# Performance work log

Hardware: AMD Instinct MI355X
Metric: run time of the kernel (lower is better)

The kernel has to match this reference:

```python
import jax, jax.numpy as jnp
import numpy as np

EMBED_DIM = 1024
NUM_HEADS = 16
HEAD_DIM = EMBED_DIM // NUM_HEADS


def setup_inputs() -> dict:
    key = jax.random.key(0)
    ks = jax.random.split(key, 9)
    s = 1.0 / np.sqrt(EMBED_DIM)
    inp = {"x": jax.random.normal(ks[0], (2, 2048, EMBED_DIM), dtype=jnp.float32)}
    for i, name in enumerate(["q", "k", "v", "out"]):
        inp[f"W_{name}"] = jax.random.uniform(ks[1 + 2 * i], (EMBED_DIM, EMBED_DIM), jnp.float32, -s, s)
        inp[f"b_{name}"] = jax.random.uniform(ks[2 + 2 * i], (EMBED_DIM,), jnp.float32, -s, s)
    return inp


def _heads(x):
    # [B, S, D] -> [B, H, S, Dh]
    b, s, _ = x.shape
    return x.reshape(b, s, NUM_HEADS, HEAD_DIM).transpose(0, 2, 1, 3)


def reference(x, W_q, b_q, W_k, b_k, W_v, b_v, W_out, b_out):
    q = _heads(x @ W_q.T + b_q)
    k = _heads(x @ W_k.T + b_k)
    v = _heads(x @ W_v.T + b_v)
    scale = HEAD_DIM ** 0.5
    logits = jnp.einsum("bhqd,bhkd->bhqk", q, k) / scale  # [B,H,S,S]
    s = x.shape[1]
    causal = jnp.tril(jnp.ones((s, s), dtype=bool))
    logits = jnp.where(causal, logits, -jnp.inf)
    a = jax.nn.softmax(logits, axis=-1)
    o = jnp.einsum("bhqk,bhkd->bhqd", a, v)
    o = o.transpose(0, 2, 1, 3).reshape(x.shape[0], s, EMBED_DIM)
    return o @ W_out.T + b_out
```

## Files before the change

### kernel.cpp

```cpp
#include <hip/hip_runtime.h>
#include <hip/hip_bf16.h>

typedef __bf16 bf16_t;
typedef __bf16 bf16x8 __attribute__((ext_vector_type(8)));
typedef __bf16 bf16x4 __attribute__((ext_vector_type(4)));
typedef float  f32x4  __attribute__((ext_vector_type(4)));

#define MFMA16(a, b, c) __builtin_amdgcn_mfma_f32_16x16x32_bf16((a), (b), (c), 0, 0, 0)

constexpr int E  = 1024;
constexpr int S  = 2048;
constexpr int H  = 16;
constexpr int M  = 4096;

__device__ __forceinline__ void glds16(const bf16_t* src, bf16_t* dst) {
  __builtin_amdgcn_global_load_lds(
      (const __attribute__((address_space(1))) void*)src,
      (__attribute__((address_space(3))) void*)dst, 16, 0, 0);
}

template <int ROWS, int NT>
__device__ __forceinline__ void stage_tile(const bf16_t* g, int gld,
                                           bf16_t* lds, int tid) {
  const int w = tid >> 6, l = tid & 63;
#pragma unroll
  for (int i = 0; i < ROWS * 8 / NT; ++i) {
    const int c = i * NT + w * 64 + l;
    const int row = c >> 3;
    const int gch = (c & 7) ^ (row & 7);
    glds16(g + (size_t)row * gld + gch * 8, lds + (size_t)(i * NT + w * 64) * 8);
  }
}

__device__ __forceinline__ bf16x8 read_frag(const bf16_t* lds, int row, int kc) {
  return *(const bf16x8*)(lds + (size_t)((row << 3) + (kc ^ (row & 7))) * 8);
}

__global__ void cvt_all_kernel(const float* __restrict__ x,
                               const float* __restrict__ w0, const float* __restrict__ w1,
                               const float* __restrict__ w2, const float* __restrict__ w3,
                               bf16_t* __restrict__ xb,
                               bf16_t* __restrict__ o0, bf16_t* __restrict__ o1,
                               bf16_t* __restrict__ o2, bf16_t* __restrict__ o3) {
  const int bid = blockIdx.x;
  const float* s;
  bf16_t* d;
  int idx;
  if (bid < 4096) {
    s = x; d = xb; idx = bid * 256 + threadIdx.x;
  } else {
    const int seg = (bid - 4096) >> 10;
    s = seg == 0 ? w0 : seg == 1 ? w1 : seg == 2 ? w2 : w3;
    d = seg == 0 ? o0 : seg == 1 ? o1 : seg == 2 ? o2 : o3;
    idx = ((bid - 4096) & 1023) * 256 + threadIdx.x;
  }
  float4 v = ((const float4*)s)[idx];
  bf16x4 o;
  o[0] = (bf16_t)v.x; o[1] = (bf16_t)v.y; o[2] = (bf16_t)v.z; o[3] = (bf16_t)v.w;
  ((bf16x4*)d)[idx] = o;
}

__device__ __forceinline__ void gemm_core(const bf16_t* __restrict__ A,
                                          const bf16_t* __restrict__ W, int Kd,
                                          bf16_t* As, bf16_t* Bs, int tid,
                                          f32x4 acc[4][4]) {
  const int w = tid >> 6, l = tid & 63;
  const int lq = l & 15, qd = l >> 4;
  const int wr = (w >> 1) * 64, wc = (w & 1) * 64;
#pragma unroll
  for (int i = 0; i < 4; ++i)
#pragma unroll
    for (int j = 0; j < 4; ++j) acc[i][j] = (f32x4){0.f, 0.f, 0.f, 0.f};

  const int KT = Kd / 64;
  for (int kt = 0; kt < KT; ++kt) {
    __syncthreads();
    stage_tile<128, 256>(A + kt * 64, Kd, As, tid);
    stage_tile<128, 256>(W + kt * 64, Kd, Bs, tid);
    __syncthreads();
#pragma unroll
    for (int ks = 0; ks < 2; ++ks) {
      bf16x8 af[4], bw[4];
#pragma unroll
      for (int mi = 0; mi < 4; ++mi)
        af[mi] = read_frag(As, wr + mi * 16 + lq, ks * 4 + qd);
#pragma unroll
      for (int ni = 0; ni < 4; ++ni)
        bw[ni] = read_frag(Bs, wc + ni * 16 + lq, ks * 4 + qd);
#pragma unroll
      for (int mi = 0; mi < 4; ++mi)
#pragma unroll
        for (int ni = 0; ni < 4; ++ni)
          acc[mi][ni] = MFMA16(af[mi], bw[ni], acc[mi][ni]);
    }
  }
}

__global__ __launch_bounds__(256) void qkv_gemm_kernel(
    const bf16_t* __restrict__ xb,
    const bf16_t* __restrict__ wq, const bf16_t* __restrict__ wk,
    const bf16_t* __restrict__ wv,
    const float* __restrict__ bq, const float* __restrict__ bk,
    const float* __restrict__ bv,
    bf16_t* __restrict__ Qb, bf16_t* __restrict__ Kb, bf16_t* __restrict__ Vb) {
  __shared__ __align__(16) bf16_t As[128 * 64];
  __shared__ __align__(16) bf16_t Bs[128 * 64];
  const int tid = threadIdx.x;
  const int which = blockIdx.x >> 3;
  const int n0 = (blockIdx.x & 7) * 128;
  const int m0 = blockIdx.y * 128;
  const bf16_t* Wp = which == 0 ? wq : which == 1 ? wk : wv;
  const float* bp  = which == 0 ? bq : which == 1 ? bk : bv;
  bf16_t* Out      = which == 0 ? Qb : which == 1 ? Kb : Vb;
  const float sc = (which == 0) ? (1.4426950408889634f * 0.125f) : 1.0f;

  f32x4 acc[4][4];
  gemm_core(xb + (size_t)m0 * E, Wp + (size_t)n0 * E, E, As, Bs, tid, acc);

  const int w = tid >> 6, l = tid & 63, lq = l & 15, qd = l >> 4;
  const int wr = (w >> 1) * 64, wc = (w & 1) * 64;
#pragma unroll
  for (int ni = 0; ni < 4; ++ni) {
    const int col = n0 + wc + ni * 16 + lq;
    const float bvv = bp[col];
#pragma unroll
    for (int mi = 0; mi < 4; ++mi)
#pragma unroll
      for (int r = 0; r < 4; ++r) {
        const int row = m0 + wr + mi * 16 + qd * 4 + r;
        Out[(size_t)row * E + col] = (bf16_t)((acc[mi][ni][r] + bvv) * sc);
      }
  }
}

__global__ __launch_bounds__(256) void vtrans_kernel(const bf16_t* __restrict__ Vb,
                                                     bf16_t* __restrict__ VT) {
  constexpr int LDT = 72;
  __shared__ __align__(16) bf16_t T[64 * LDT];
  const int tid = threadIdx.x;
  const int st = blockIdx.x, bh = blockIdx.y;
  const int b = bh >> 4, h = bh & 15;
  const int s0 = st * 64;
  const size_t rowbase = (size_t)b * S;
#pragma unroll
  for (int i = 0; i < 2; ++i) {
    const int c = i * 256 + tid;
    const int sl = c >> 3, dp = c & 7;
    const int p = (sl & 15) * 4 + (sl >> 4);
    bf16x8 v = *(const bf16x8*)(Vb + (rowbase + s0 + sl) * E + h * 64 + dp * 8);
    *(bf16x8*)&T[p * LDT + dp * 8] = v;
  }
  __syncthreads();
#pragma unroll
  for (int i = 0; i < 2; ++i) {
    const int c = i * 256 + tid;
    const int d = c >> 3, pp = (c & 7) * 8;
    bf16x8 o;
#pragma unroll
    for (int j = 0; j < 8; ++j) o[j] = T[(pp + j) * LDT + d];
    *(bf16x8*)&VT[((size_t)bh * 64 + d) * S + s0 + pp] = o;
  }
}

__global__ __launch_bounds__(256) void oproj_gemm_kernel(
    const bf16_t* __restrict__ Ob, const bf16_t* __restrict__ wo,
    const float* __restrict__ bo, float* __restrict__ out) {
  __shared__ __align__(16) bf16_t As[64 * 64];
  __shared__ __align__(16) bf16_t Bs[128 * 64];
  const int tid = threadIdx.x;
  const int n0 = blockIdx.x * 128;
  const int m0 = blockIdx.y * 64;
  const int w = tid >> 6, l = tid & 63, lq = l & 15, qd = l >> 4;
  const int wr = (w >> 1) * 32, wc = (w & 1) * 64;

  f32x4 acc[2][4];
#pragma unroll
  for (int i = 0; i < 2; ++i)
#pragma unroll
    for (int j = 0; j < 4; ++j) acc[i][j] = (f32x4){0.f, 0.f, 0.f, 0.f};

  for (int kt = 0; kt < 16; ++kt) {
    __syncthreads();
    stage_tile<64, 256>(Ob + (size_t)m0 * E + kt * 64, E, As, tid);
    stage_tile<128, 256>(wo + (size_t)n0 * E + kt * 64, E, Bs, tid);
    __syncthreads();
#pragma unroll
    for (int ks = 0; ks < 2; ++ks) {
      bf16x8 af[2], bw[4];
#pragma unroll
      for (int mi = 0; mi < 2; ++mi)
        af[mi] = read_frag(As, wr + mi * 16 + lq, ks * 4 + qd);
#pragma unroll
      for (int ni = 0; ni < 4; ++ni)
        bw[ni] = read_frag(Bs, wc + ni * 16 + lq, ks * 4 + qd);
#pragma unroll
      for (int mi = 0; mi < 2; ++mi)
#pragma unroll
        for (int ni = 0; ni < 4; ++ni)
          acc[mi][ni] = MFMA16(af[mi], bw[ni], acc[mi][ni]);
    }
  }
#pragma unroll
  for (int ni = 0; ni < 4; ++ni) {
    const int col = n0 + wc + ni * 16 + lq;
    const float bvv = bo[col];
#pragma unroll
    for (int mi = 0; mi < 2; ++mi)
#pragma unroll
      for (int r = 0; r < 4; ++r) {
        const int row = m0 + wr + mi * 16 + qd * 4 + r;
        out[(size_t)row * E + col] = acc[mi][ni][r] + bvv;
      }
  }
}

__global__ __launch_bounds__(256, 3) void attn_kernel(
    const bf16_t* __restrict__ Q, const bf16_t* __restrict__ K,
    const bf16_t* __restrict__ VT, bf16_t* __restrict__ O,
    unsigned int* __restrict__ counter) {
  constexpr int LDP = 72;
  __shared__ __align__(16) bf16_t Ks[64 * 64];
  __shared__ __align__(16) bf16_t Vt[64 * 64];
  __shared__ __align__(16) bf16_t Ps[4][16 * LDP];
  __shared__ int item_sh;

  const int tid = threadIdx.x;
  const int w = tid >> 6, l = tid & 63;
  const int lq = l & 15, qd = l >> 4;

  for (;;) {
    if (tid == 0) item_sh = (int)atomicAdd(counter, 1u);
    __syncthreads();
    const int item = item_sh;
    if (item >= 1024) break;
    const int qt = 31 - (item >> 5);
    const int bh = item & 31;
    const int b = bh >> 4, h = bh & 15;
    const int q0 = qt * 64;
    const int qr = q0 + w * 16;
    const size_t rowbase = (size_t)b * S;
    const size_t vtbase = (size_t)bh * 64 * S;

    bf16x8 aq[2];
#pragma unroll
    for (int ks = 0; ks < 2; ++ks)
      aq[ks] = *(const bf16x8*)(Q + (rowbase + qr + lq) * E + h * 64 + ks * 32 + qd * 8);

    f32x4 oacc[4];
#pragma unroll
    for (int nt = 0; nt < 4; ++nt) oacc[nt] = (f32x4){0.f, 0.f, 0.f, 0.f};
    float rs[4] = {0.f, 0.f, 0.f, 0.f};

    for (int kt = 0; kt <= qt; ++kt) {
      const int k0 = kt * 64;
      __syncthreads();
      stage_tile<64, 256>(K + (rowbase + k0) * E + h * 64, E, Ks, tid);
      stage_tile<64, 256>(VT + vtbase + k0, S, Vt, tid);
      __syncthreads();

      const bool needmask = (k0 + 63 > qr);
      f32x4 sacc[4];
#pragma unroll
      for (int nt = 0; nt < 4; ++nt) sacc[nt] = (f32x4){0.f, 0.f, 0.f, 0.f};
#pragma unroll
      for (int ks = 0; ks < 2; ++ks) {
        bf16x8 bk[4];
#pragma unroll
        for (int nt = 0; nt < 4; ++nt)
          bk[nt] = read_frag(Ks, nt * 16 + lq, ks * 4 + qd);
#pragma unroll
        for (int nt = 0; nt < 4; ++nt)
          sacc[nt] = MFMA16(aq[ks], bk[nt], sacc[nt]);
      }
#pragma unroll
      for (int r = 0; r < 4; ++r) {
        bf16x4 pk;
#pragma unroll
        for (int nt = 0; nt < 4; ++nt) {
          float pv = exp2f(sacc[nt][r]);
          if (needmask) {
            const int kg = k0 + nt * 16 + lq;
            const int qg = qr + qd * 4 + r;
            pv = (kg > qg) ? 0.f : pv;
          }
          rs[r] += pv;
          pk[nt] = (bf16_t)pv;
        }
        *(bf16x4*)&Ps[w][(qd * 4 + r) * LDP + lq * 4] = pk;
      }
      bf16x8 ap[2];
#pragma unroll
      for (int ks = 0; ks < 2; ++ks)
        ap[ks] = *(const bf16x8*)&Ps[w][lq * LDP + ks * 32 + qd * 8];
#pragma unroll
      for (int ks = 0; ks < 2; ++ks) {
        bf16x8 bv[4];
#pragma unroll
        for (int nt = 0; nt < 4; ++nt)
          bv[nt] = read_frag(Vt, nt * 16 + lq, ks * 4 + qd);
#pragma unroll
        for (int nt = 0; nt < 4; ++nt)
          oacc[nt] = MFMA16(ap[ks], bv[nt], oacc[nt]);
      }
    }

    float rinv[4];
#pragma unroll
    for (int r = 0; r < 4; ++r) {
      float t = rs[r];
      t += __shfl_xor(t, 1);
      t += __shfl_xor(t, 2);
      t += __shfl_xor(t, 4);
      t += __shfl_xor(t, 8);
      rinv[r] = 1.0f / t;
    }
#pragma unroll
    for (int nt = 0; nt < 4; ++nt)
#pragma unroll
      for (int r = 0; r < 4; ++r) {
        const int qg = qr + qd * 4 + r;
        O[(rowbase + qg) * E + h * 64 + nt * 16 + lq] =
            (bf16_t)(oacc[nt][r] * rinv[r]);
      }
  }
}

extern "C" void kernel_launch(void* const* d_in, const int* in_sizes, int n_in,
                              void* d_out, int out_size, void* d_ws, size_t ws_size,
                              hipStream_t stream) {
  const float* x  = (const float*)d_in[0];
  const float* Wq = (const float*)d_in[1];
  const float* bq = (const float*)d_in[2];
  const float* Wk = (const float*)d_in[3];
  const float* bk = (const float*)d_in[4];
  const float* Wv = (const float*)d_in[5];
  const float* bv = (const float*)d_in[6];
  const float* Wo = (const float*)d_in[7];
  const float* bo = (const float*)d_in[8];
  float* out = (float*)d_out;

  unsigned char* ws = (unsigned char*)d_ws;
  constexpr size_t MB = 1ull << 20;
  bf16_t* xb  = (bf16_t*)(ws + 0 * MB);
  bf16_t* wqb = (bf16_t*)(ws + 8 * MB);
  bf16_t* wkb = (bf16_t*)(ws + 10 * MB);
  bf16_t* wvb = (bf16_t*)(ws + 12 * MB);
  bf16_t* wob = (bf16_t*)(ws + 14 * MB);
  bf16_t* Qb  = (bf16_t*)(ws + 16 * MB);
  bf16_t* Kb  = (bf16_t*)(ws + 24 * MB);
  bf16_t* Vb  = (bf16_t*)(ws + 32 * MB);
  bf16_t* VT  = (bf16_t*)(ws + 40 * MB);
  bf16_t* Ob  = xb;
  unsigned int* counter = (unsigned int*)(ws + 32 * MB);

  cvt_all_kernel<<<4096 + 4 * 1024, 256, 0, stream>>>(
      x, Wq, Wk, Wv, Wo, xb, wqb, wkb, wvb, wob);

  qkv_gemm_kernel<<<dim3(24, 32), 256, 0, stream>>>(
      xb, wqb, wkb, wvb, bq, bk, bv, Qb, Kb, Vb);

  vtrans_kernel<<<dim3(32, 32), 256, 0, stream>>>(Vb, VT);

  hipMemsetAsync(counter, 0, sizeof(unsigned int), stream);

  attn_kernel<<<768, 256, 0, stream>>>(Qb, Kb, VT, Ob, counter);

  oproj_gemm_kernel<<<dim3(8, 64), 256, 0, stream>>>(Ob, wob, bo, out);
}
```

Measured before the change: 210.1 us.

## Split long causal attention rows across key chunks with atomic combine; shrink GEMM tiles

Query tiles with many key blocks are split into up to three 12-block key chunks. Partial unnormalised outputs and row sums are accumulated with float atomics into a zeroed fp32 buffer, and a new combine kernel normalises them. The goal is to balance the causal workload and raise parallelism. The QKV and output-projection GEMMs also use smaller tiles to launch more blocks. The costs are a large memset, atomic traffic, an extra kernel launch, and workspace aliasing that now reuses the xb and Vb regions.

```diff
diff --git a/kernel.cpp b/kernel.cpp
--- a/kernel.cpp
+++ b/kernel.cpp
@@ -60,42 +60,6 @@
   ((bf16x4*)d)[idx] = o;
 }
 
-__device__ __forceinline__ void gemm_core(const bf16_t* __restrict__ A,
-                                          const bf16_t* __restrict__ W, int Kd,
-                                          bf16_t* As, bf16_t* Bs, int tid,
-                                          f32x4 acc[4][4]) {
-  const int w = tid >> 6, l = tid & 63;
-  const int lq = l & 15, qd = l >> 4;
-  const int wr = (w >> 1) * 64, wc = (w & 1) * 64;
-#pragma unroll
-  for (int i = 0; i < 4; ++i)
-#pragma unroll
-    for (int j = 0; j < 4; ++j) acc[i][j] = (f32x4){0.f, 0.f, 0.f, 0.f};
-
-  const int KT = Kd / 64;
-  for (int kt = 0; kt < KT; ++kt) {
-    __syncthreads();
-    stage_tile<128, 256>(A + kt * 64, Kd, As, tid);
-    stage_tile<128, 256>(W + kt * 64, Kd, Bs, tid);
-    __syncthreads();
-#pragma unroll
-    for (int ks = 0; ks < 2; ++ks) {
-      bf16x8 af[4], bw[4];
-#pragma unroll
-      for (int mi = 0; mi < 4; ++mi)
-        af[mi] = read_frag(As, wr + mi * 16 + lq, ks * 4 + qd);
-#pragma unroll
-      for (int ni = 0; ni < 4; ++ni)
-        bw[ni] = read_frag(Bs, wc + ni * 16 + lq, ks * 4 + qd);
-#pragma unroll
-      for (int mi = 0; mi < 4; ++mi)
-#pragma unroll
-        for (int ni = 0; ni < 4; ++ni)
-          acc[mi][ni] = MFMA16(af[mi], bw[ni], acc[mi][ni]);
-    }
-  }
-}
-
 __global__ __launch_bounds__(256) void qkv_gemm_kernel(
     const bf16_t* __restrict__ xb,
     const bf16_t* __restrict__ wq, const bf16_t* __restrict__ wk,
@@ -103,28 +67,53 @@
     const float* __restrict__ bq, const float* __restrict__ bk,
     const float* __restrict__ bv,
     bf16_t* __restrict__ Qb, bf16_t* __restrict__ Kb, bf16_t* __restrict__ Vb) {
-  __shared__ __align__(16) bf16_t As[128 * 64];
+  __shared__ __align__(16) bf16_t As[64 * 64];
   __shared__ __align__(16) bf16_t Bs[128 * 64];
   const int tid = threadIdx.x;
   const int which = blockIdx.x >> 3;
   const int n0 = (blockIdx.x & 7) * 128;
-  const int m0 = blockIdx.y * 128;
+  const int m0 = blockIdx.y * 64;
   const bf16_t* Wp = which == 0 ? wq : which == 1 ? wk : wv;
   const float* bp  = which == 0 ? bq : which == 1 ? bk : bv;
   bf16_t* Out      = which == 0 ? Qb : which == 1 ? Kb : Vb;
   const float sc = (which == 0) ? (1.4426950408889634f * 0.125f) : 1.0f;
 
-  f32x4 acc[4][4];
-  gemm_core(xb + (size_t)m0 * E, Wp + (size_t)n0 * E, E, As, Bs, tid, acc);
-
   const int w = tid >> 6, l = tid & 63, lq = l & 15, qd = l >> 4;
-  const int wr = (w >> 1) * 64, wc = (w & 1) * 64;
+  const int wr = (w >> 1) * 32, wc = (w & 1) * 64;
+
+  f32x4 acc[2][4];
+#pragma unroll
+  for (int i = 0; i < 2; ++i)
+#pragma unroll
+    for (int j = 0; j < 4; ++j) acc[i][j] = (f32x4){0.f, 0.f, 0.f, 0.f};
+
+  for (int kt = 0; kt < 16; ++kt) {
+    __syncthreads();
+    stage_tile<64, 256>(xb + (size_t)m0 * E + kt * 64, E, As, tid);
+    stage_tile<128, 256>(Wp + (size_t)n0 * E + kt * 64, E, Bs, tid);
+    __syncthreads();
+#pragma unroll
+    for (int ks = 0; ks < 2; ++ks) {
+      bf16x8 af[2], bw[4];
+#pragma unroll
+      for (int mi = 0; mi < 2; ++mi)
+        af[mi] = read_frag(As, wr + mi * 16 + lq, ks * 4 + qd);
+#pragma unroll
+      for (int ni = 0; ni < 4; ++ni)
+        bw[ni] = read_frag(Bs, wc + ni * 16 + lq, ks * 4 + qd);
+#pragma unroll
+      for (int mi = 0; mi < 2; ++mi)
+#pragma unroll
+        for (int ni = 0; ni < 4; ++ni)
+          acc[mi][ni] = MFMA16(af[mi], bw[ni], acc[mi][ni]);
+    }
+  }
 #pragma unroll
   for (int ni = 0; ni < 4; ++ni) {
     const int col = n0 + wc + ni * 16 + lq;
     const float bvv = bp[col];
 #pragma unroll
-    for (int mi = 0; mi < 4; ++mi)
+    for (int mi = 0; mi < 2; ++mi)
 #pragma unroll
       for (int r = 0; r < 4; ++r) {
         const int row = m0 + wr + mi * 16 + qd * 4 + r;
@@ -166,42 +155,42 @@
     const bf16_t* __restrict__ Ob, const bf16_t* __restrict__ wo,
     const float* __restrict__ bo, float* __restrict__ out) {
   __shared__ __align__(16) bf16_t As[64 * 64];
-  __shared__ __align__(16) bf16_t Bs[128 * 64];
+  __shared__ __align__(16) bf16_t Bs[64 * 64];
   const int tid = threadIdx.x;
-  const int n0 = blockIdx.x * 128;
+  const int n0 = blockIdx.x * 64;
   const int m0 = blockIdx.y * 64;
   const int w = tid >> 6, l = tid & 63, lq = l & 15, qd = l >> 4;
-  const int wr = (w >> 1) * 32, wc = (w & 1) * 64;
-
-  f32x4 acc[2][4];
+  const int wr = (w >> 1) * 32, wc = (w & 1) * 32;
+
+  f32x4 acc[2][2];
 #pragma unroll
   for (int i = 0; i < 2; ++i)
 #pragma unroll
-    for (int j = 0; j < 4; ++j) acc[i][j] = (f32x4){0.f, 0.f, 0.f, 0.f};
+    for (int j = 0; j < 2; ++j) acc[i][j] = (f32x4){0.f, 0.f, 0.f, 0.f};
 
   for (int kt = 0; kt < 16; ++kt) {
     __syncthreads();
     stage_tile<64, 256>(Ob + (size_t)m0 * E + kt * 64, E, As, tid);
-    stage_tile<128, 256>(wo + (size_t)n0 * E + kt * 64, E, Bs, tid);
+    stage_tile<64, 256>(wo + (size_t)n0 * E + kt * 64, E, Bs, tid);
     __syncthreads();
 #pragma unroll
     for (int ks = 0; ks < 2; ++ks) {
-      bf16x8 af[2], bw[4];
+      bf16x8 af[2], bw[2];
 #pragma unroll
       for (int mi = 0; mi < 2; ++mi)
         af[mi] = read_frag(As, wr + mi * 16 + lq, ks * 4 + qd);
 #pragma unroll
-      for (int ni = 0; ni < 4; ++ni)
+      for (int ni = 0; ni < 2; ++ni)
         bw[ni] = read_frag(Bs, wc + ni * 16 + lq, ks * 4 + qd);
 #pragma unroll
       for (int mi = 0; mi < 2; ++mi)
 #pragma unroll
-        for (int ni = 0; ni < 4; ++ni)
+        for (int ni = 0; ni < 2; ++ni)
           acc[mi][ni] = MFMA16(af[mi], bw[ni], acc[mi][ni]);
     }
   }
 #pragma unroll
-  for (int ni = 0; ni < 4; ++ni) {
+  for (int ni = 0; ni < 2; ++ni) {
     const int col = n0 + wc + ni * 16 + lq;
     const float bvv = bo[col];
 #pragma unroll
@@ -217,6 +206,7 @@
 __global__ __launch_bounds__(256, 3) void attn_kernel(
     const bf16_t* __restrict__ Q, const bf16_t* __restrict__ K,
     const bf16_t* __restrict__ VT, bf16_t* __restrict__ O,
+    float* __restrict__ O32, float* __restrict__ RS,
     unsigned int* __restrict__ counter) {
   constexpr int LDP = 72;
   __shared__ __align__(16) bf16_t Ks[64 * 64];
@@ -232,14 +222,22 @@
     if (tid == 0) item_sh = (int)atomicAdd(counter, 1u);
     __syncthreads();
     const int item = item_sh;
-    if (item >= 1024) break;
-    const int qt = 31 - (item >> 5);
-    const int bh = item & 31;
+    if (item >= 1920) break;
+    const int bh = item / 60;
+    const int j = item - bh * 60;
+    int qt, ck;
+    if (j < 24)      { const int t = j / 3;        qt = 31 - t; ck = j - t * 3; }
+    else if (j < 48) { const int t = j - 24;       qt = 23 - (t >> 1); ck = t & 1; }
+    else             {                             qt = 59 - j; ck = 0; }
+    const int klo = ck * 12;
+    const int khi = (klo + 12 < qt + 1) ? (klo + 12) : (qt + 1);
+
     const int b = bh >> 4, h = bh & 15;
     const int q0 = qt * 64;
     const int qr = q0 + w * 16;
     const size_t rowbase = (size_t)b * S;
     const size_t vtbase = (size_t)bh * 64 * S;
+    const bf16_t* Kg = K + rowbase * E + h * 64;
 
     bf16x8 aq[2];
 #pragma unroll
@@ -251,10 +249,10 @@
     for (int nt = 0; nt < 4; ++nt) oacc[nt] = (f32x4){0.f, 0.f, 0.f, 0.f};
     float rs[4] = {0.f, 0.f, 0.f, 0.f};
 
-    for (int kt = 0; kt <= qt; ++kt) {
+    for (int kt = klo; kt < khi; ++kt) {
       const int k0 = kt * 64;
       __syncthreads();
-      stage_tile<64, 256>(K + (rowbase + k0) * E + h * 64, E, Ks, tid);
+      stage_tile<64, 256>(Kg + (size_t)k0 * E, E, Ks, tid);
       stage_tile<64, 256>(VT + vtbase + k0, S, Vt, tid);
       __syncthreads();
 
@@ -304,7 +302,7 @@
       }
     }
 
-    float rinv[4];
+    float rt[4];
 #pragma unroll
     for (int r = 0; r < 4; ++r) {
       float t = rs[r];
@@ -312,17 +310,50 @@
       t += __shfl_xor(t, 2);
       t += __shfl_xor(t, 4);
       t += __shfl_xor(t, 8);
-      rinv[r] = 1.0f / t;
+      rt[r] = t;
     }
-#pragma unroll
-    for (int nt = 0; nt < 4; ++nt)
-#pragma unroll
-      for (int r = 0; r < 4; ++r) {
-        const int qg = qr + qd * 4 + r;
-        O[(rowbase + qg) * E + h * 64 + nt * 16 + lq] =
-            (bf16_t)(oacc[nt][r] * rinv[r]);
-      }
-  }
+
+    if (qt < 12) {
+#pragma unroll
+      for (int nt = 0; nt < 4; ++nt)
+#pragma unroll
+        for (int r = 0; r < 4; ++r) {
+          const int qg = qr + qd * 4 + r;
+          O[(rowbase + qg) * E + h * 64 + nt * 16 + lq] =
+              (bf16_t)(oacc[nt][r] / rt[r]);
+        }
+    } else {
+#pragma unroll
+      for (int nt = 0; nt < 4; ++nt)
+#pragma unroll
+        for (int r = 0; r < 4; ++r) {
+          const int qg = qr + qd * 4 + r;
+          atomicAdd(&O32[((size_t)(b * 1280 + qg - 768) << 10) + h * 64 + nt * 16 + lq],
+                    oacc[nt][r]);
+        }
+      if (lq == 0) {
+#pragma unroll
+        for (int r = 0; r < 4; ++r) {
+          const int qg = qr + qd * 4 + r;
+          atomicAdd(&RS[bh * 1280 + qg - 768], rt[r]);
+        }
+      }
+    }
+  }
+}
+
+__global__ __launch_bounds__(256) void combine_kernel(
+    const float* __restrict__ O32, const float* __restrict__ RS,
+    bf16_t* __restrict__ O) {
+  const int qloc = blockIdx.x, b = blockIdx.y;
+  const int col = threadIdx.x * 4;
+  const int h = col >> 6;
+  const float4 v = *(const float4*)&O32[((size_t)(b * 1280 + qloc) << 10) + col];
+  const float rinv = 1.0f / RS[(b * 16 + h) * 1280 + qloc];
+  bf16x4 o;
+  o[0] = (bf16_t)(v.x * rinv); o[1] = (bf16_t)(v.y * rinv);
+  o[2] = (bf16_t)(v.z * rinv); o[3] = (bf16_t)(v.w * rinv);
+  *(bf16x4*)&O[((size_t)(b * 2048 + 768 + qloc)) * E + col] = o;
 }
 
 extern "C" void kernel_launch(void* const* d_in, const int* in_sizes, int n_in,
@@ -350,20 +381,24 @@
   bf16_t* Kb  = (bf16_t*)(ws + 24 * MB);
   bf16_t* Vb  = (bf16_t*)(ws + 32 * MB);
   bf16_t* VT  = (bf16_t*)(ws + 40 * MB);
-  bf16_t* Ob  = xb;
-  unsigned int* counter = (unsigned int*)(ws + 32 * MB);
+  float*  O32 = (float*)(ws + 0 * MB);
+  float*  RS  = (float*)(ws + 10 * MB);
+  unsigned int* counter = (unsigned int*)(ws + 10 * MB + 160 * 1024);
+  bf16_t* Ob  = Vb;
 
   cvt_all_kernel<<<4096 + 4 * 1024, 256, 0, stream>>>(
       x, Wq, Wk, Wv, Wo, xb, wqb, wkb, wvb, wob);
 
-  qkv_gemm_kernel<<<dim3(24, 32), 256, 0, stream>>>(
+  qkv_gemm_kernel<<<dim3(24, 64), 256, 0, stream>>>(
       xb, wqb, wkb, wvb, bq, bk, bv, Qb, Kb, Vb);
 
   vtrans_kernel<<<dim3(32, 32), 256, 0, stream>>>(Vb, VT);
 
-  hipMemsetAsync(counter, 0, sizeof(unsigned int), stream);
-
-  attn_kernel<<<768, 256, 0, stream>>>(Qb, Kb, VT, Ob, counter);
-
-  oproj_gemm_kernel<<<dim3(8, 64), 256, 0, stream>>>(Ob, wob, bo, out);
-}
+  hipMemsetAsync(ws, 0, 10 * MB + 160 * 1024 + 64, stream);
+
+  attn_kernel<<<1536, 256, 0, stream>>>(Qb, Kb, VT, Ob, O32, RS, counter);
+
+  combine_kernel<<<dim3(1280, 2), 256, 0, stream>>>(O32, RS, Ob);
+
+  oproj_gemm_kernel<<<dim3(16, 64), 256, 0, stream>>>(Ob, wob, bo, out);
+}
```

Result: slower. 216.7 us (+3.2%).
